# Kernel optimization log

Measured on AMD Instinct MI355X. Metric: run time of the kernel, lower is better.

## Reference

```python
import jax, jax.numpy as jnp
import numpy as np

T = 17            # tensor side -> 289 flat channels
C = T * T
EPS = 1e-5


def tconv(x, W1, W2, b, stride):
    """Tucker-2 tensor conv: per offset (i,j) OUT = W1[i,j] @ X @ W2[i,j].
    x: [B, a*bt, H, W]; W1: [kh,kw,T,a]; W2: [kh,kw,bt,T]; b: [289].
    Equivalent dense kernel K[(p,q),(a,b),i,j] = W1[i,j,p,a]*W2[i,j,b,q]."""
    kh, kw, _, a = W1.shape
    bt = W2.shape[2]
    K = jnp.einsum('ijpa,ijbq->pqabij', W1, W2).reshape(C, a * bt, kh, kw)
    pad = (kh - 1) // 2
    y = jax.lax.conv_general_dilated(
        x, K, (stride, stride), [(pad, pad), (pad, pad)],
        dimension_numbers=('NCHW', 'OIHW', 'NCHW'))
    return y + b.reshape(1, C, 1, 1)


def bn(x, g, bta):
    # training-mode BN over flattened 17x17 tensor channels (biased var)
    m = jnp.mean(x, axis=(0, 2, 3), keepdims=True)
    v = jnp.var(x, axis=(0, 2, 3), keepdims=True)
    return g.reshape(1, -1, 1, 1) * (x - m) * jax.lax.rsqrt(v + EPS) + bta.reshape(1, -1, 1, 1)


def prelu(x, a):
    return jnp.where(x >= 0, x, a * x)


def setup_inputs() -> dict:
    key = jax.random.key(0)
    ks = jax.random.split(key, 8)
    x = jax.random.normal(ks[0], (32, 3, 160, 160), dtype=jnp.float32)
    s = 0.1
    feat_W1 = jax.random.normal(ks[1], (3, 3, T, 3), dtype=jnp.float32) * s
    feat_W2 = jax.random.normal(ks[2], (3, 3, 1, T), dtype=jnp.float32) * s
    feat_b = jnp.zeros((C,), dtype=jnp.float32)
    # 27 1x1 convs: shortcuts 0..8, block k uses 9+2k and 10+2k
    c11_W1 = jax.random.normal(ks[3], (27, 1, 1, T, T), dtype=jnp.float32) * s
    c11_W2 = jax.random.normal(ks[4], (27, 1, 1, T, T), dtype=jnp.float32) * s
    c11_b = jnp.zeros((27, C), dtype=jnp.float32)
    # 9 3x3 convs (one per block)
    c33_W1 = jax.random.normal(ks[5], (9, 3, 3, T, T), dtype=jnp.float32) * s
    c33_W2 = jax.random.normal(ks[6], (9, 3, 3, T, T), dtype=jnp.float32) * s
    c33_b = jnp.zeros((9, C), dtype=jnp.float32)
    # 37 BNs: 0=features, 1+j shortcut j, 10+3k..12+3k block k
    bn_g = jnp.ones((37, C), dtype=jnp.float32)
    bn_bt = jnp.zeros((37, C), dtype=jnp.float32)
    # 19 PReLUs: 0=features, block k uses 1+2k, 2+2k
    prelu_a = jnp.full((19,), 0.25, dtype=jnp.float32)
    return {"x": x, "feat_W1": feat_W1, "feat_W2": feat_W2, "feat_b": feat_b,
            "c11_W1": c11_W1, "c11_W2": c11_W2, "c11_b": c11_b,
            "c33_W1": c33_W1, "c33_W2": c33_W2, "c33_b": c33_b,
            "bn_g": bn_g, "bn_bt": bn_bt, "prelu_a": prelu_a}


def reference(x, feat_W1, feat_W2, feat_b, c11_W1, c11_W2, c11_b,
              c33_W1, c33_W2, c33_b, bn_g, bn_bt, prelu_a):
    # features: 3x3 s2 tensor conv [3,1]->[17,17], BN, PReLU
    h = tconv(x, feat_W1, feat_W2, feat_b, 2)
    h = prelu(bn(h, bn_g[0], bn_bt[0]), prelu_a[0])
    # 9 residual blocks; blocks 0,1 downsample by 2
    for k in range(9):
        s = 2 if k < 2 else 1
        i1, i2 = 9 + 2 * k, 10 + 2 * k
        j = 10 + 3 * k
        idn = bn(tconv(h, c11_W1[k], c11_W2[k], c11_b[k], s), bn_g[1 + k], bn_bt[1 + k])
        y = prelu(bn(tconv(h, c11_W1[i1], c11_W2[i1], c11_b[i1], 1), bn_g[j], bn_bt[j]), prelu_a[1 + 2 * k])
        y = prelu(bn(tconv(y, c33_W1[k], c33_W2[k], c33_b[k], s), bn_g[j + 1], bn_bt[j + 1]), prelu_a[2 + 2 * k])
        y = bn(tconv(y, c11_W1[i2], c11_W2[i2], c11_b[i2], 1), bn_g[j + 2], bn_bt[j + 2])
        h = y + idn
    return h  # [B, 289, 20, 20] == torch [B,1,20,20,17,17] flattened
```

## Files before the change

### kernel.cpp

```cpp
#include <hip/hip_runtime.h>
#include <hip/hip_bf16.h>

#define EPS 1e-5f
#define NB 256
#define CSTR 292
#define PST 580

typedef __hip_bfloat16 bf16;
typedef short s16x8 __attribute__((ext_vector_type(8)));
typedef float f32x4 __attribute__((ext_vector_type(4)));
typedef unsigned short u16x4 __attribute__((ext_vector_type(4)));
typedef unsigned short u16x8 __attribute__((ext_vector_type(8)));

__device__ inline float bf2f(unsigned short u) {
    union { unsigned int i; float f; } z; z.i = ((unsigned int)u) << 16; return z.f;
}
__device__ inline unsigned short f2bf(float f) {
    union { bf16 h; unsigned short u; } z; z.h = __float2bfloat16(f); return z.u;
}
__device__ inline unsigned short f2bf_trunc(float f) {
    union { float f; unsigned int u; } z; z.f = f; return (unsigned short)(z.u >> 16);
}
__device__ inline float ldv(const bf16* p, long i) { return __bfloat162float(p[i]); }
__device__ inline float ldv(const float* p, long i) { return p[i]; }

__device__ __forceinline__ void prep_frag(const float* w1, const float* w2,
                                          bf16* o, int kt, int nt, int l) {
#pragma unroll
    for (int e = 0; e < 8; ++e) {
        int k = kt * 32 + ((l >> 4) << 3) + e;
        int n = nt * 16 + (l & 15);
        float v = 0.f;
        if (k < 289 && n < 289)
            v = w1[(n / 17) * 17 + (k / 17)] * w2[(k % 17) * 17 + (n % 17)];
        o[e] = __float2bfloat16(v);
    }
}

__global__ void prep11_all_k(const float* __restrict__ W1all, const float* __restrict__ W2all,
                             bf16* __restrict__ Bsw) {
    int bi = blockIdx.x;
    int cv = bi / 190, r = bi - cv * 190;
    int kt = r / 19, nt = r - kt * 19;
    prep_frag(W1all + (size_t)cv * 289, W2all + (size_t)cv * 289,
              Bsw + (size_t)bi * 512 + threadIdx.x * 8, kt, nt, threadIdx.x);
}

__global__ void prep33_k(const float* __restrict__ W1, const float* __restrict__ W2,
                         bf16* __restrict__ Bsw) {
    int bi = blockIdx.x;
    int tap = bi / 190; int r = bi - tap * 190;
    int kt = r / 19, nt = r - kt * 19;
    prep_frag(W1 + (size_t)tap * 289, W2 + (size_t)tap * 289,
              Bsw + (size_t)bi * 512 + threadIdx.x * 8, kt, nt, threadIdx.x);
}

__global__ void feat_k(const float* __restrict__ x, bf16* __restrict__ out,
                       const float* __restrict__ W1, const float* __restrict__ W2) {
    __shared__ float W1s[459], W2s[153];
    int tid = threadIdx.x;
    for (int i = tid; i < 459; i += 256) W1s[i] = W1[i];
    for (int i = tid; i < 153; i += 256) W2s[i] = W2[i];
    __syncthreads();
    const long N = 204800L * 17;
    for (long idx = (long)blockIdx.x * 256 + tid; idx < N; idx += 524288L) {
        int pix = (int)(idx / 17), p = (int)(idx - (long)pix * 17);
        int b = pix / 6400; int rr = pix - b * 6400;
        int oh = rr / 80, ow = rr - oh * 80;
        float y[17];
#pragma unroll
        for (int q = 0; q < 17; ++q) y[q] = 0.f;
        for (int di = 0; di < 3; ++di) {
            int ih = oh * 2 + di - 1;
            if (ih < 0 || ih >= 160) continue;
            for (int dj = 0; dj < 3; ++dj) {
                int iw = ow * 2 + dj - 1;
                if (iw < 0 || iw >= 160) continue;
                int k = di * 3 + dj;
                long xb = (long)b * 76800 + ih * 160 + iw;
                float dot = W1s[(k * 17 + p) * 3 + 0] * x[xb]
                          + W1s[(k * 17 + p) * 3 + 1] * x[xb + 25600]
                          + W1s[(k * 17 + p) * 3 + 2] * x[xb + 51200];
#pragma unroll
                for (int q = 0; q < 17; ++q) y[q] += dot * W2s[k * 17 + q];
            }
        }
        long op = (long)pix * CSTR + p * 17;
#pragma unroll
        for (int q = 0; q < 17; ++q) out[op + q] = __float2bfloat16(y[q]);
    }
}

template <typename TI, typename TO, int TAPS, bool DUAL, int MT>
__global__ __launch_bounds__(256, MT == 2 ? 3 : 5) void gemm_k(
    const TI* __restrict__ in1, const TI* __restrict__ in2, TO* __restrict__ out,
    const bf16* __restrict__ Bs, const float* __restrict__ scshAll, int bn1, int bn2,
    const float* __restrict__ alphaPtr, float* __restrict__ partial,
    int Hin, int Win, int Hout, int Wout, int stride) {
    constexpr int MROWS = 16 * MT;
    constexpr int SITS = (37 * MROWS + 255) / 256;
    static_assert(MROWS * 304 * sizeof(TO) <= 2 * MROWS * 640, "epilogue must fit As");
    __shared__ char As[2 * MROWS * 640];
    __shared__ float sc1[296], sh1[296];
    __shared__ float sc2[DUAL ? 296 : 1], sh2[DUAL ? 296 : 1];
    __shared__ long gb00[MROWS];
    __shared__ int ihw0[MROWS];
    int tid = threadIdx.x;
    int HWin = Hin * Win, HWout = Hout * Wout;
    int pix0 = blockIdx.x * MROWS;
    for (int i = tid; i < 296; i += 256) {
        int cc = i < 289 ? i : 0;
        sc1[i] = scshAll[bn1 * 578 + cc]; sh1[i] = scshAll[bn1 * 578 + 289 + cc];
        if constexpr (DUAL) {
            sc2[i] = scshAll[bn2 * 578 + cc]; sh2[i] = scshAll[bn2 * 578 + 289 + cc];
        }
    }
    if (tid < MROWS) {
        int op = pix0 + tid;
        int b = op / HWout; int rr = op - b * HWout;
        int oh = rr / Wout, ow = rr - oh * Wout;
        int ih0 = oh * stride + (TAPS == 9 ? -1 : 0);
        int iw0 = ow * stride + (TAPS == 9 ? -1 : 0);
        gb00[tid] = ((long)b * HWin + (long)ih0 * Win + iw0) * CSTR;
        ihw0[tid] = ((ih0 + 1) << 16) | (iw0 + 1);
    }
    if (tid < 8 * MROWS) {
        int half = tid / (4 * MROWS), r = (tid >> 2) & (MROWS - 1), c = tid & 3;
        int byte = (r * 640 + 576 + c * 16) ^ ((r & 7) << 4);
        *(u16x8*)(As + half * (MROWS * 640) + byte) = (u16x8){0, 0, 0, 0, 0, 0, 0, 0};
    }
    float alpha = DUAL ? 0.f : *alphaPtr;
    int w = tid >> 6, l = tid & 63;
    int nt0 = w * 5;
    int lane_n = l & 15;
    int kbyte = (l >> 4) << 4;
    f32x4 acc[MT][5];
#pragma unroll
    for (int m = 0; m < MT; ++m)
#pragma unroll
        for (int j = 0; j < 5; ++j) acc[m][j] = (f32x4){0.f, 0.f, 0.f, 0.f};
    __syncthreads();

    bool cact[SITS]; int cih[SITS], ciw[SITS], cwb[SITS], ck0[SITS]; long cgb[SITS];
#pragma unroll
    for (int it = 0; it < SITS; ++it) {
        int cid = it * 256 + tid;
        cact[it] = cid < 37 * MROWS;
        int row = cact[it] ? cid / 37 : 0;
        int j = cid - row * 37;
        ck0[it] = j * 8;
        cgb[it] = gb00[row] + j * 8;
        int pk = ihw0[row];
        cih[it] = (pk >> 16) - 1; ciw[it] = (pk & 0xffff) - 1;
        cwb[it] = (row * 640 + j * 16) ^ ((row & 7) << 4);
    }
    bool vld[SITS];
    u16x4 rh1[SITS][2]; f32x4 rf1[SITS][2];
    u16x4 rh2[DUAL ? SITS : 1][2]; f32x4 rf2[DUAL ? SITS : 1][2];

    auto LOAD = [&](int tap) {
        int di = (TAPS == 9) ? tap / 3 : 0;
        int dj = (TAPS == 9) ? tap - di * 3 : 0;
        long toff = (long)(di * Win + dj) * CSTR;
#pragma unroll
        for (int it = 0; it < SITS; ++it) {
            vld[it] = false;
            if (cact[it]) {
                int ih = cih[it] + di, iw = ciw[it] + dj;
                if (ih >= 0 && ih < Hin && iw >= 0 && iw < Win) {
                    vld[it] = true;
                    long gb = cgb[it] + toff;
                    if constexpr (sizeof(TI) == 2) {
                        rh1[it][0] = *(const u16x4*)((const bf16*)in1 + gb);
                        rh1[it][1] = *(const u16x4*)((const bf16*)in1 + gb + 4);
                        if constexpr (DUAL) {
                            rh2[it][0] = *(const u16x4*)((const bf16*)in2 + gb);
                            rh2[it][1] = *(const u16x4*)((const bf16*)in2 + gb + 4);
                        }
                    } else {
                        rf1[it][0] = *(const f32x4*)((const float*)in1 + gb);
                        rf1[it][1] = *(const f32x4*)((const float*)in1 + gb + 4);
                        if constexpr (DUAL) {
                            rf2[it][0] = *(const f32x4*)((const float*)in2 + gb);
                            rf2[it][1] = *(const f32x4*)((const float*)in2 + gb + 4);
                        }
                    }
                }
            }
        }
    };

    auto WRITE = [&]() {
#pragma unroll
        for (int it = 0; it < SITS; ++it) {
            if (!cact[it]) continue;
            float v[8];
            if (vld[it]) {
                int k0 = ck0[it];
                float r[8];
                if constexpr (sizeof(TI) == 2) {
#pragma unroll
                    for (int e = 0; e < 4; ++e) {
                        r[e] = bf2f(rh1[it][0][e]); r[4 + e] = bf2f(rh1[it][1][e]);
                    }
                } else {
#pragma unroll
                    for (int e = 0; e < 4; ++e) {
                        r[e] = rf1[it][0][e]; r[4 + e] = rf1[it][1][e];
                    }
                }
#pragma unroll
                for (int e = 0; e < 8; ++e) v[e] = sc1[k0 + e] * r[e] + sh1[k0 + e];
                if constexpr (DUAL) {
                    float q[8];
                    if constexpr (sizeof(TI) == 2) {
#pragma unroll
                        for (int e = 0; e < 4; ++e) {
                            q[e] = bf2f(rh2[it][0][e]); q[4 + e] = bf2f(rh2[it][1][e]);
                        }
                    } else {
#pragma unroll
                        for (int e = 0; e < 4; ++e) {
                            q[e] = rf2[it][0][e]; q[4 + e] = rf2[it][1][e];
                        }
                    }
#pragma unroll
                    for (int e = 0; e < 8; ++e) v[e] += sc2[k0 + e] * q[e] + sh2[k0 + e];
                } else {
#pragma unroll
                    for (int e = 0; e < 8; ++e) v[e] = v[e] >= 0.f ? v[e] : alpha * v[e];
                }
#pragma unroll
                for (int e = 0; e < 8; ++e) if (ck0[it] + e > 288) v[e] = 0.f;
            } else {
#pragma unroll
                for (int e = 0; e < 8; ++e) v[e] = 0.f;
            }
            u16x4 hi0, hi1, lo0, lo1;
#pragma unroll
            for (int e = 0; e < 4; ++e) {
                unsigned short h = f2bf(v[e]);
                hi0[e] = h; lo0[e] = f2bf_trunc(v[e] - bf2f(h));
                unsigned short h2 = f2bf(v[4 + e]);
                hi1[e] = h2; lo1[e] = f2bf_trunc(v[4 + e] - bf2f(h2));
            }
            int byte = cwb[it];
            *(u16x4*)(As + byte) = hi0;
            *(u16x4*)(As + byte + 8) = hi1;
            *(u16x4*)(As + MROWS * 640 + byte) = lo0;
            *(u16x4*)(As + MROWS * 640 + byte + 8) = lo1;
        }
    };

    LOAD(0);
#pragma unroll 1
    for (int tap = 0; tap < TAPS; ++tap) {
        WRITE();
        if (tap + 1 < TAPS) LOAD(tap + 1);
        __syncthreads();
        const bf16* bp = Bs + (size_t)tap * 97280 + (size_t)l * 8;
        int swz = (lane_n & 7) << 4;
        __builtin_amdgcn_s_setprio(1);
#pragma unroll 2
        for (int kt = 0; kt < 10; ++kt) {
            s16x8 ah[MT], al[MT];
#pragma unroll
            for (int m = 0; m < MT; ++m) {
                int ro = ((m * 16 + lane_n) * 640 + kbyte + kt * 64) ^ swz;
                ah[m] = *(const s16x8*)(As + ro);
                al[m] = *(const s16x8*)(As + MROWS * 640 + ro);
            }
#pragma unroll
            for (int j = 0; j < 5; ++j) {
                if (j < 4 || w < 3) {
                    s16x8 bfr = *(const s16x8*)(bp + (size_t)(kt * 19 + nt0 + j) * 512);
#pragma unroll
                    for (int m = 0; m < MT; ++m) {
                        acc[m][j] = __builtin_amdgcn_mfma_f32_16x16x32_bf16(
                            ah[m], bfr, acc[m][j], 0, 0, 0);
                        acc[m][j] = __builtin_amdgcn_mfma_f32_16x16x32_bf16(
                            al[m], bfr, acc[m][j], 0, 0, 0);
                    }
                }
            }
        }
        __builtin_amdgcn_s_setprio(0);
        __syncthreads();
    }
    {
#pragma unroll
        for (int j = 0; j < 5; ++j) {
            float s = 0.f, ss = 0.f;
            if (j < 4 || w < 3) {
#pragma unroll
                for (int m = 0; m < MT; ++m)
#pragma unroll
                    for (int e = 0; e < 4; ++e) {
                        float v = acc[m][j][e];
                        s += v; ss += v * v;
                    }
            }
            s += __shfl_xor(s, 16); ss += __shfl_xor(ss, 16);
            s += __shfl_xor(s, 32); ss += __shfl_xor(ss, 32);
            int n = (nt0 + j) * 16 + lane_n;
            if (l < 16 && n < 289 && (j < 4 || w < 3)) {
                partial[(long)blockIdx.x * PST + n] = s;
                partial[(long)blockIdx.x * PST + 290 + n] = ss;
            }
        }
    }
    {
        TO* ep = (TO*)As;
        int re = (l >> 4) << 2;
#pragma unroll
        for (int m = 0; m < MT; ++m) {
#pragma unroll
            for (int j = 0; j < 5; ++j) {
                if (j < 4 || w < 3) {
                    int n = (nt0 + j) * 16 + lane_n;
#pragma unroll
                    for (int e = 0; e < 4; ++e) {
                        if constexpr (sizeof(TO) == 2)
                            ep[(m * 16 + re + e) * 304 + n] = __float2bfloat16(acc[m][j][e]);
                        else
                            ((float*)ep)[(m * 16 + re + e) * 304 + n] = acc[m][j][e];
                    }
                }
            }
        }
        __syncthreads();
        for (int cid = tid; cid < MROWS * 73; cid += 256) {
            int row = cid / 73, j = cid - row * 73;
            long g = (long)(pix0 + row) * CSTR + j * 4;
            if constexpr (sizeof(TO) == 2) {
                u16x4 v = *(const u16x4*)((const bf16*)ep + row * 304 + j * 4);
                *(u16x4*)((bf16*)out + g) = v;
            } else {
                f32x4 v = *(const f32x4*)((const float*)ep + row * 304 + j * 4);
                *(f32x4*)((float*)out + g) = v;
            }
        }
    }
}

__global__ __launch_bounds__(256, 3) void gemm2_k(
    const float* __restrict__ in1, const float* __restrict__ in2,
    float* __restrict__ out1, float* __restrict__ out2,
    const bf16* __restrict__ Bs1, const bf16* __restrict__ Bs2,
    const float* __restrict__ scshAll, int bn1, int bn2,
    float* __restrict__ partial1, float* __restrict__ partial2) {
    constexpr int MROWS = 16;
    __shared__ char As[2 * MROWS * 640];
    __shared__ float sc1[296], sh1[296], sc2[296], sh2[296];
    int tid = threadIdx.x;
    for (int i = tid; i < 296; i += 256) {
        int cc = i < 289 ? i : 0;
        sc1[i] = scshAll[bn1 * 578 + cc]; sh1[i] = scshAll[bn1 * 578 + 289 + cc];
        sc2[i] = scshAll[bn2 * 578 + cc]; sh2[i] = scshAll[bn2 * 578 + 289 + cc];
    }
    if (tid < 128) {
        int half = tid >> 6, r = (tid >> 2) & 15, c = tid & 3;
        int byte = (r * 640 + 576 + c * 16) ^ ((r & 7) << 4);
        *(u16x8*)(As + half * (MROWS * 640) + byte) = (u16x8){0, 0, 0, 0, 0, 0, 0, 0};
    }
    int pix0 = blockIdx.x * MROWS;
    int w = tid >> 6, l = tid & 63;
    int nt0 = w * 5, lane_n = l & 15, kbyte = (l >> 4) << 4;
    f32x4 acc1[5], acc2[5];
#pragma unroll
    for (int j = 0; j < 5; ++j) {
        acc1[j] = (f32x4){0.f, 0.f, 0.f, 0.f};
        acc2[j] = (f32x4){0.f, 0.f, 0.f, 0.f};
    }
    __syncthreads();
#pragma unroll
    for (int it = 0; it < 3; ++it) {
        int cid = it * 256 + tid;
        if (cid < 592) {
            int row = cid / 37, j = cid - row * 37, k0 = j * 8;
            long gb = (long)(pix0 + row) * CSTR + k0;
            f32x4 a = *(const f32x4*)(in1 + gb), b = *(const f32x4*)(in1 + gb + 4);
            f32x4 c = *(const f32x4*)(in2 + gb), d = *(const f32x4*)(in2 + gb + 4);
            float v[8];
#pragma unroll
            for (int e = 0; e < 4; ++e) {
                v[e] = sc1[k0 + e] * a[e] + sh1[k0 + e] + sc2[k0 + e] * c[e] + sh2[k0 + e];
                v[4 + e] = sc1[k0 + 4 + e] * b[e] + sh1[k0 + 4 + e]
                         + sc2[k0 + 4 + e] * d[e] + sh2[k0 + 4 + e];
            }
#pragma unroll
            for (int e = 0; e < 8; ++e) if (k0 + e > 288) v[e] = 0.f;
            u16x4 hi0, hi1, lo0, lo1;
#pragma unroll
            for (int e = 0; e < 4; ++e) {
                unsigned short h = f2bf(v[e]);
                hi0[e] = h; lo0[e] = f2bf_trunc(v[e] - bf2f(h));
                unsigned short h2 = f2bf(v[4 + e]);
                hi1[e] = h2; lo1[e] = f2bf_trunc(v[4 + e] - bf2f(h2));
            }
            int byte = (row * 640 + j * 16) ^ ((row & 7) << 4);
            *(u16x4*)(As + byte) = hi0;
            *(u16x4*)(As + byte + 8) = hi1;
            *(u16x4*)(As + MROWS * 640 + byte) = lo0;
            *(u16x4*)(As + MROWS * 640 + byte + 8) = lo1;
        }
    }
    __syncthreads();
    const bf16* bp1 = Bs1 + (size_t)l * 8;
    const bf16* bp2 = Bs2 + (size_t)l * 8;
    int swz = (lane_n & 7) << 4;
    __builtin_amdgcn_s_setprio(1);
#pragma unroll 2
    for (int kt = 0; kt < 10; ++kt) {
        int ro = (lane_n * 640 + kbyte + kt * 64) ^ swz;
        s16x8 ah = *(const s16x8*)(As + ro);
        s16x8 al = *(const s16x8*)(As + MROWS * 640 + ro);
#pragma unroll
        for (int j = 0; j < 5; ++j) {
            if (j < 4 || w < 3) {
                size_t fo = (size_t)(kt * 19 + nt0 + j) * 512;
                s16x8 b1 = *(const s16x8*)(bp1 + fo);
                acc1[j] = __builtin_amdgcn_mfma_f32_16x16x32_bf16(ah, b1, acc1[j], 0, 0, 0);
                acc1[j] = __builtin_amdgcn_mfma_f32_16x16x32_bf16(al, b1, acc1[j], 0, 0, 0);
                s16x8 b2 = *(const s16x8*)(bp2 + fo);
                acc2[j] = __builtin_amdgcn_mfma_f32_16x16x32_bf16(ah, b2, acc2[j], 0, 0, 0);
                acc2[j] = __builtin_amdgcn_mfma_f32_16x16x32_bf16(al, b2, acc2[j], 0, 0, 0);
            }
        }
    }
    __builtin_amdgcn_s_setprio(0);
    __syncthreads();
#pragma unroll
    for (int j = 0; j < 5; ++j) {
        float s1 = 0.f, q1 = 0.f, s2 = 0.f, q2 = 0.f;
        if (j < 4 || w < 3) {
#pragma unroll
            for (int e = 0; e < 4; ++e) {
                float v1 = acc1[j][e]; s1 += v1; q1 += v1 * v1;
                float v2 = acc2[j][e]; s2 += v2; q2 += v2 * v2;
            }
        }
        s1 += __shfl_xor(s1, 16); q1 += __shfl_xor(q1, 16);
        s1 += __shfl_xor(s1, 32); q1 += __shfl_xor(q1, 32);
        s2 += __shfl_xor(s2, 16); q2 += __shfl_xor(q2, 16);
        s2 += __shfl_xor(s2, 32); q2 += __shfl_xor(q2, 32);
        int n = (nt0 + j) * 16 + lane_n;
        if (l < 16 && n < 289 && (j < 4 || w < 3)) {
            partial1[(long)blockIdx.x * PST + n] = s1;
            partial1[(long)blockIdx.x * PST + 290 + n] = q1;
            partial2[(long)blockIdx.x * PST + n] = s2;
            partial2[(long)blockIdx.x * PST + 290 + n] = q2;
        }
    }
    float* ep = (float*)As;
    int re = (l >> 4) << 2;
#pragma unroll
    for (int pass = 0; pass < 2; ++pass) {
        const f32x4* ac = pass ? acc2 : acc1;
        float* op = pass ? out2 : out1;
#pragma unroll
        for (int j = 0; j < 5; ++j) {
            if (j < 4 || w < 3) {
                int n = (nt0 + j) * 16 + lane_n;
#pragma unroll
                for (int e = 0; e < 4; ++e) ep[(re + e) * 304 + n] = ac[j][e];
            }
        }
        __syncthreads();
        for (int cid = tid; cid < MROWS * 73; cid += 256) {
            int row = cid / 73, j = cid - row * 73;
            long g = (long)(pix0 + row) * CSTR + j * 4;
            f32x4 v = *(const f32x4*)(ep + row * 304 + j * 4);
            *(f32x4*)(op + g) = v;
        }
        __syncthreads();
    }
}

__global__ void stats_k(const bf16* __restrict__ t, float* __restrict__ partial, int npix) {
    int c = threadIdx.x;
    if (c >= 289) return;
    float s = 0.f, ss = 0.f;
    for (int pix = blockIdx.x; pix < npix; pix += NB) {
        float v = ldv(t, (long)pix * CSTR + c);
        s += v; ss += v * v;
    }
    partial[(long)blockIdx.x * PST + c] = s;
    partial[(long)blockIdx.x * PST + 290 + c] = ss;
}

__device__ __forceinline__ void fin_one(const float* partial, const float* g,
                                        const float* bt, float* scshAll,
                                        int bnid, float invN, int GN, int c) {
    float s = 0.f, ss = 0.f;
    for (int k = threadIdx.x; k < GN; k += 256) {
        s += partial[(long)k * PST + c];
        ss += partial[(long)k * PST + 290 + c];
    }
    for (int o = 32; o; o >>= 1) { s += __shfl_down(s, o); ss += __shfl_down(ss, o); }
    __shared__ float ls[4], lss[4];
    int w = threadIdx.x >> 6;
    if ((threadIdx.x & 63) == 0) { ls[w] = s; lss[w] = ss; }
    __syncthreads();
    if (threadIdx.x == 0) {
        s = ls[0] + ls[1] + ls[2] + ls[3];
        ss = lss[0] + lss[1] + lss[2] + lss[3];
        float m = s * invN;
        float v = ss * invN - m * m;
        float sc = g[c] * rsqrtf(v + EPS);
        scshAll[bnid * 578 + c] = sc;
        scshAll[bnid * 578 + 289 + c] = bt[c] - m * sc;
    }
}

__global__ void finalize_k(const float* __restrict__ partial, const float* __restrict__ g,
                           const float* __restrict__ bt, float* __restrict__ scshAll,
                           int bnid, float invN, int GN) {
    fin_one(partial, g, bt, scshAll, bnid, invN, GN, blockIdx.x);
}

__global__ void finalize2_k(const float* __restrict__ pA, const float* __restrict__ pB,
                            const float* __restrict__ gAll, const float* __restrict__ btAll,
                            float* __restrict__ scshAll, int bnA, int bnB,
                            float invN, int GN) {
    int q = blockIdx.x / 289, c = blockIdx.x - q * 289;
    const float* p = q ? pB : pA;
    int bnid = q ? bnB : bnA;
    fin_one(p, gAll + bnid * 289, btAll + bnid * 289, scshAll, bnid, invN, GN, c);
}

__global__ void final_k(const float* __restrict__ y3, const float* __restrict__ idn,
                        float* __restrict__ out, const float* __restrict__ scshAll,
                        int bnY, int bnI) {
    __shared__ float T[32][305];
    int bi = blockIdx.x;
    int b = bi / 13, t0 = (bi - (bi / 13) * 13) * 32;
    int tid = threadIdx.x;
    int nhw = 400 - t0; if (nhw > 32) nhw = 32;
    for (int idx = tid; idx < 32 * 304; idx += 256) {
        int hwl = idx / 304, c = idx - hwl * 304;
        float v = 0.f;
        if (hwl < nhw && c < 289) {
            long pix = (long)b * 400 + t0 + hwl;
            v = scshAll[bnY * 578 + c] * y3[pix * CSTR + c] + scshAll[bnY * 578 + 289 + c]
              + scshAll[bnI * 578 + c] * idn[pix * CSTR + c] + scshAll[bnI * 578 + 289 + c];
        }
        T[hwl][c] = v;
    }
    __syncthreads();
    for (int idx = tid; idx < 289 * 32; idx += 256) {
        int c = idx >> 5, hwl = idx & 31;
        if (hwl < nhw)
            out[((long)b * 289 + c) * 400 + t0 + hwl] = T[hwl][c];
    }
}

extern "C" void kernel_launch(void* const* d_in, const int* in_sizes, int n_in,
                              void* d_out, int out_size, void* d_ws, size_t ws_size,
                              hipStream_t stream) {
    const float* x     = (const float*)d_in[0];
    const float* fW1   = (const float*)d_in[1];
    const float* fW2   = (const float*)d_in[2];
    const float* c11W1 = (const float*)d_in[4];
    const float* c11W2 = (const float*)d_in[5];
    const float* c33W1 = (const float*)d_in[7];
    const float* c33W2 = (const float*)d_in[8];
    const float* bng   = (const float*)d_in[10];
    const float* bnbt  = (const float*)d_in[11];
    const float* pa    = (const float*)d_in[12];
    float* outp = (float*)d_out;

    char* base = (char*)d_ws;
    bf16*  A    = (bf16*)base;
    bf16*  Bb   = (bf16*)(base + 119603200L);
    bf16*  Cb   = (bf16*)(base + 149504000L);
    float* scsh = (float*)(base + 179404800L);
    bf16*  B33s = (bf16*)(base + 179490368L);
    size_t need = 181241408L;
    if (ws_size < need) return;
    float* D = (float*)base;
    float* E = (float*)(base + 14950400L);
    float* F = (float*)(base + 29900800L);

    float* partial = (float*)d_out;
    bf16*  B11all  = (bf16*)((char*)d_out + 7424000L);
    float* partial2 = partial + 800L * PST;
    float* partialBig = (float*)Cb;

    const float inv80 = 1.f / 204800.f, inv40 = 1.f / 51200.f, inv20 = 1.f / 12800.f;

#define B11(cv) (B11all + (size_t)(cv) * 97280)
#define PREP33(cv) prep33_k<<<dim3(1710), dim3(64), 0, stream>>>( \
        c33W1 + (long)(cv) * 9 * 289, c33W2 + (long)(cv) * 9 * 289, B33s)
#define FIN(P, bnid, invN, GN) finalize_k<<<dim3(289), dim3(256), 0, stream>>>( \
        (P), bng + (bnid) * 289, bnbt + (bnid) * 289, scsh, (bnid), (invN), (GN))

    prep11_all_k<<<dim3(27 * 190), dim3(64), 0, stream>>>(c11W1, c11W2, B11all);

    feat_k<<<dim3(2048), dim3(256), 0, stream>>>(x, A, fW1, fW2);
    stats_k<<<dim3(NB), dim3(320), 0, stream>>>(A, partial, 204800);
    FIN(partial, 0, inv80, NB);

    gemm_k<bf16, bf16, 1, false, 2><<<dim3(1600), dim3(256), 0, stream>>>(
        A, nullptr, Bb, B11(0), scsh, 0, 0, pa + 0, partial, 80, 80, 40, 40, 2);
    FIN(partial, 1, inv40, 1600);
    gemm_k<bf16, bf16, 1, false, 2><<<dim3(6400), dim3(256), 0, stream>>>(
        A, nullptr, A, B11(9), scsh, 0, 0, pa + 0, partialBig, 80, 80, 80, 80, 1);
    FIN(partialBig, 10, inv80, 6400);
    PREP33(0);
    gemm_k<bf16, bf16, 9, false, 2><<<dim3(1600), dim3(256), 0, stream>>>(
        A, nullptr, Cb, B33s, scsh, 10, 0, pa + 1, partial, 80, 80, 40, 40, 2);
    FIN(partial, 11, inv40, 1600);
    gemm_k<bf16, bf16, 1, false, 2><<<dim3(1600), dim3(256), 0, stream>>>(
        Cb, nullptr, Cb, B11(10), scsh, 11, 0, pa + 2, partial, 40, 40, 40, 40, 1);
    FIN(partial, 12, inv40, 1600);

    gemm_k<bf16, float, 1, true, 1><<<dim3(800), dim3(256), 0, stream>>>(
        Cb, Bb, D, B11(1), scsh, 12, 1, nullptr, partial, 40, 40, 20, 20, 2);
    FIN(partial, 2, inv20, 800);
    gemm_k<bf16, bf16, 1, true, 2><<<dim3(1600), dim3(256), 0, stream>>>(
        Cb, Bb, Cb, B11(11), scsh, 12, 1, nullptr, partial, 40, 40, 40, 40, 1);
    FIN(partial, 13, inv40, 1600);
    PREP33(1);
    gemm_k<bf16, float, 9, false, 2><<<dim3(400), dim3(256), 0, stream>>>(
        Cb, nullptr, E, B33s, scsh, 13, 0, pa + 3, partial, 40, 40, 20, 20, 2);
    FIN(partial, 14, inv20, 400);
    gemm_k<float, float, 1, false, 1><<<dim3(800), dim3(256), 0, stream>>>(
        E, nullptr, E, B11(12), scsh, 14, 0, pa + 4, partial, 20, 20, 20, 20, 1);
    FIN(partial, 15, inv20, 800);

    float *X = E, *Y = D, *Z = F;
    for (int k = 2; k < 9; ++k) {
        gemm2_k<<<dim3(800), dim3(256), 0, stream>>>(
            X, Y, Z, X, B11(k), B11(9 + 2 * k), scsh, 9 + 3 * k, k, partial, partial2);
        finalize2_k<<<dim3(578), dim3(256), 0, stream>>>(
            partial, partial2, bng, bnbt, scsh, 1 + k, 10 + 3 * k, inv20, 800);
        PREP33(k);
        gemm_k<float, float, 9, false, 2><<<dim3(400), dim3(256), 0, stream>>>(
            X, nullptr, Y, B33s, scsh, 10 + 3 * k, 0, pa + 1 + 2 * k, partial,
            20, 20, 20, 20, 1);
        FIN(partial, 11 + 3 * k, inv20, 400);
        gemm_k<float, float, 1, false, 1><<<dim3(800), dim3(256), 0, stream>>>(
            Y, nullptr, Y, B11(10 + 2 * k), scsh, 11 + 3 * k, 0, pa + 2 + 2 * k, partial,
            20, 20, 20, 20, 1);
        FIN(partial, 12 + 3 * k, inv20, 800);
        float* t = X; X = Y; Y = Z; Z = t;
    }
    final_k<<<dim3(416), dim3(256), 0, stream>>>(X, Y, outp, scsh, 36, 9);
}
```

Baseline: 2.278 ms.

## Batch 3x3 weight prep, merge BN finalizes, and double grid for 20x20 3x3 convs

Precomputes the swizzled bf16 fragments for the eight remaining 3x3 convs in a single launch, placed after the first 3x3 GEMM, so the per-block prep launches go away. Pairs of BN finalize launches are merged through a variant kernel that takes a separate count and partial-sum count for each BN, and the first shortcut's partials go to a separate buffer so they can be finalized alongside the next stats. The 20x20 3x3 GEMMs switch their last template argument from 2 to 1 and double their grid from 400 to 800 blocks. This gives more parallelism and fewer launches, at the cost of more workspace and more partial-sum rows for finalize to reduce.

Result: slower. 2.724 ms (+19.6%).

```diff
diff --git a/kernel.cpp b/kernel.cpp
--- a/kernel.cpp
+++ b/kernel.cpp
@@ -53,6 +53,17 @@
     int kt = r / 19, nt = r - kt * 19;
     prep_frag(W1 + (size_t)tap * 289, W2 + (size_t)tap * 289,
               Bsw + (size_t)bi * 512 + threadIdx.x * 8, kt, nt, threadIdx.x);
+}
+
+__global__ void prep33all_k(const float* __restrict__ W1, const float* __restrict__ W2,
+                            bf16* __restrict__ Bsw) {
+    int bi = blockIdx.x;
+    int kb = bi / 1710, r = bi - kb * 1710;
+    int tap = r / 190; int rr = r - tap * 190;
+    int kt = rr / 19, nt = rr - kt * 19;
+    const float* w1 = W1 + (long)(kb + 1) * 9 * 289 + (long)tap * 289;
+    const float* w2 = W2 + (long)(kb + 1) * 9 * 289 + (long)tap * 289;
+    prep_frag(w1, w2, Bsw + (size_t)bi * 512 + threadIdx.x * 8, kt, nt, threadIdx.x);
 }
 
 __global__ void feat_k(const float* __restrict__ x, bf16* __restrict__ out,
@@ -519,14 +530,15 @@
     fin_one(partial, g, bt, scshAll, bnid, invN, GN, blockIdx.x);
 }
 
-__global__ void finalize2_k(const float* __restrict__ pA, const float* __restrict__ pB,
-                            const float* __restrict__ gAll, const float* __restrict__ btAll,
-                            float* __restrict__ scshAll, int bnA, int bnB,
-                            float invN, int GN) {
+__global__ void finalize2v_k(const float* __restrict__ pA, const float* __restrict__ pB,
+                             const float* __restrict__ gAll, const float* __restrict__ btAll,
+                             float* __restrict__ scshAll, int bnA, int bnB,
+                             float invA, int GNa, float invB, int GNb) {
     int q = blockIdx.x / 289, c = blockIdx.x - q * 289;
     const float* p = q ? pB : pA;
     int bnid = q ? bnB : bnA;
-    fin_one(p, gAll + bnid * 289, btAll + bnid * 289, scshAll, bnid, invN, GN, c);
+    fin_one(p, gAll + bnid * 289, btAll + bnid * 289, scshAll, bnid,
+            q ? invB : invA, q ? GNb : GNa, c);
 }
 
 __global__ void final_k(const float* __restrict__ y3, const float* __restrict__ idn,
@@ -581,6 +593,8 @@
     float* D = (float*)base;
     float* E = (float*)(base + 14950400L);
     float* F = (float*)(base + 29900800L);
+    float* partialA = (float*)(base + 50000000L);
+    bf16*  B33all   = (bf16*)(base + 100000000L);
 
     float* partial = (float*)d_out;
     bf16*  B11all  = (bf16*)((char*)d_out + 7424000L);
@@ -590,8 +604,7 @@
     const float inv80 = 1.f / 204800.f, inv40 = 1.f / 51200.f, inv20 = 1.f / 12800.f;
 
 #define B11(cv) (B11all + (size_t)(cv) * 97280)
-#define PREP33(cv) prep33_k<<<dim3(1710), dim3(64), 0, stream>>>( \
-        c33W1 + (long)(cv) * 9 * 289, c33W2 + (long)(cv) * 9 * 289, B33s)
+#define B33A(cv) (B33all + (size_t)((cv) - 1) * 875520)
 #define FIN(P, bnid, invN, GN) finalize_k<<<dim3(289), dim3(256), 0, stream>>>( \
         (P), bng + (bnid) * 289, bnbt + (bnid) * 289, scsh, (bnid), (invN), (GN))
 
@@ -603,28 +616,28 @@
 
     gemm_k<bf16, bf16, 1, false, 2><<<dim3(1600), dim3(256), 0, stream>>>(
         A, nullptr, Bb, B11(0), scsh, 0, 0, pa + 0, partial, 80, 80, 40, 40, 2);
-    FIN(partial, 1, inv40, 1600);
     gemm_k<bf16, bf16, 1, false, 2><<<dim3(6400), dim3(256), 0, stream>>>(
         A, nullptr, A, B11(9), scsh, 0, 0, pa + 0, partialBig, 80, 80, 80, 80, 1);
-    FIN(partialBig, 10, inv80, 6400);
-    PREP33(0);
+    finalize2v_k<<<dim3(578), dim3(256), 0, stream>>>(
+        partial, partialBig, bng, bnbt, scsh, 1, 10, inv40, 1600, inv80, 6400);
+    prep33_k<<<dim3(1710), dim3(64), 0, stream>>>(c33W1, c33W2, B33s);
     gemm_k<bf16, bf16, 9, false, 2><<<dim3(1600), dim3(256), 0, stream>>>(
         A, nullptr, Cb, B33s, scsh, 10, 0, pa + 1, partial, 80, 80, 40, 40, 2);
+    prep33all_k<<<dim3(8 * 1710), dim3(64), 0, stream>>>(c33W1, c33W2, B33all);
     FIN(partial, 11, inv40, 1600);
     gemm_k<bf16, bf16, 1, false, 2><<<dim3(1600), dim3(256), 0, stream>>>(
         Cb, nullptr, Cb, B11(10), scsh, 11, 0, pa + 2, partial, 40, 40, 40, 40, 1);
     FIN(partial, 12, inv40, 1600);
 
     gemm_k<bf16, float, 1, true, 1><<<dim3(800), dim3(256), 0, stream>>>(
-        Cb, Bb, D, B11(1), scsh, 12, 1, nullptr, partial, 40, 40, 20, 20, 2);
-    FIN(partial, 2, inv20, 800);
+        Cb, Bb, D, B11(1), scsh, 12, 1, nullptr, partialA, 40, 40, 20, 20, 2);
     gemm_k<bf16, bf16, 1, true, 2><<<dim3(1600), dim3(256), 0, stream>>>(
         Cb, Bb, Cb, B11(11), scsh, 12, 1, nullptr, partial, 40, 40, 40, 40, 1);
-    FIN(partial, 13, inv40, 1600);
-    PREP33(1);
-    gemm_k<bf16, float, 9, false, 2><<<dim3(400), dim3(256), 0, stream>>>(
-        Cb, nullptr, E, B33s, scsh, 13, 0, pa + 3, partial, 40, 40, 20, 20, 2);
-    FIN(partial, 14, inv20, 400);
+    finalize2v_k<<<dim3(578), dim3(256), 0, stream>>>(
+        partialA, partial, bng, bnbt, scsh, 2, 13, inv20, 800, inv40, 1600);
+    gemm_k<bf16, float, 9, false, 1><<<dim3(800), dim3(256), 0, stream>>>(
+        Cb, nullptr, E, B33A(1), scsh, 13, 0, pa + 3, partial, 40, 40, 20, 20, 2);
+    FIN(partial, 14, inv20, 800);
     gemm_k<float, float, 1, false, 1><<<dim3(800), dim3(256), 0, stream>>>(
         E, nullptr, E, B11(12), scsh, 14, 0, pa + 4, partial, 20, 20, 20, 20, 1);
     FIN(partial, 15, inv20, 800);
@@ -633,13 +646,13 @@
     for (int k = 2; k < 9; ++k) {
         gemm2_k<<<dim3(800), dim3(256), 0, stream>>>(
             X, Y, Z, X, B11(k), B11(9 + 2 * k), scsh, 9 + 3 * k, k, partial, partial2);
-        finalize2_k<<<dim3(578), dim3(256), 0, stream>>>(
-            partial, partial2, bng, bnbt, scsh, 1 + k, 10 + 3 * k, inv20, 800);
-        PREP33(k);
-        gemm_k<float, float, 9, false, 2><<<dim3(400), dim3(256), 0, stream>>>(
-            X, nullptr, Y, B33s, scsh, 10 + 3 * k, 0, pa + 1 + 2 * k, partial,
+        finalize2v_k<<<dim3(578), dim3(256), 0, stream>>>(
+            partial, partial2, bng, bnbt, scsh, 1 + k, 10 + 3 * k,
+            inv20, 800, inv20, 800);
+        gemm_k<float, float, 9, false, 1><<<dim3(800), dim3(256), 0, stream>>>(
+            X, nullptr, Y, B33A(k), scsh, 10 + 3 * k, 0, pa + 1 + 2 * k, partial,
             20, 20, 20, 20, 1);
-        FIN(partial, 11 + 3 * k, inv20, 400);
+        FIN(partial, 11 + 3 * k, inv20, 800);
         gemm_k<float, float, 1, false, 1><<<dim3(800), dim3(256), 0, stream>>>(
             Y, nullptr, Y, B11(10 + 2 * k), scsh, 11 + 3 * k, 0, pa + 2 + 2 * k, partial,
             20, 20, 20, 20, 1);
```
